# Kernel optimization log

Measured on AMD Instinct MI355X. Metric: run time of the kernel, lower is better.

Reference implementation:

```python
import jax, jax.numpy as jnp
import numpy as np

TEMP = 0.07
EPS = 1e-8
NUM_CLASSES = 7
THRESH = 0.3


def setup_inputs() -> dict:
    key = jax.random.key(0)
    k1, k2, k3, k4, k5 = jax.random.split(key, 5)
    N, H, E, C = 8192, 128, 256, NUM_CLASSES
    reps = jax.random.normal(k1, (N, H), dtype=jnp.float32)
    labels = jax.random.randint(k2, (N,), 0, C, dtype=jnp.int64 if jax.config.jax_enable_x64 else jnp.int32)
    centers = jax.random.normal(k3, (C, E), dtype=jnp.float32)
    fc_w = jax.random.normal(k4, (H, E), dtype=jnp.float32) * (1.0 / np.sqrt(E))
    fc_b = jax.random.normal(k5, (H,), dtype=jnp.float32) * 0.01
    return {"reps": reps, "labels": labels, "centers": centers, "fc_w": fc_w, "fc_b": fc_b}


def reference(reps, labels, centers, fc_w, fc_b):
    # fc(default_centers): [C, H]
    curr_centers = centers @ fc_w.T + fc_b
    pad_labels = jnp.arange(NUM_CLASSES, dtype=labels.dtype)

    all_reps = jnp.concatenate([reps, curr_centers], axis=0)      # [M, H]
    all_labels = jnp.concatenate([labels, pad_labels], axis=0)    # [M]
    B = reps.shape[0]
    M = all_reps.shape[0]

    # cosine similarity via normalized matmul (avoids [B,M,H] broadcast)
    norms = jnp.sqrt(jnp.sum(all_reps * all_reps, axis=-1))
    rn = all_reps / jnp.maximum(norms, 1e-8)[:, None]
    cos = rn[:B] @ rn.T                                           # [B, M]

    scores = (1.0 + cos) * 0.5 + EPS
    eye = (jnp.arange(B)[:, None] == jnp.arange(M)[None, :]).astype(scores.dtype)
    scores = scores * (1.0 - eye) / TEMP
    # torch uses .item() on the max -> a non-differentiable constant
    scores = scores - jax.lax.stop_gradient(jnp.max(scores))
    e = jnp.exp(scores)

    pos_mask = (labels[:, None] == all_labels[None, :]).astype(scores.dtype)  # [B, M]
    mask = 1.0 - eye

    pos_sum = jnp.sum(e * pos_mask * mask, axis=-1)
    neg_sum = jnp.sum(e * (1.0 - pos_mask), axis=-1)
    probs = pos_sum / (pos_sum + neg_sum)
    probs = probs / (jnp.sum(pos_mask * mask, axis=-1) + EPS)

    loss_vec = -jnp.log(probs + EPS)
    loss_mask = (loss_vec > THRESH).astype(loss_vec.dtype)
    denom = jax.lax.stop_gradient(jnp.sum(loss_mask)) + EPS
    loss = jnp.sum(loss_vec * loss_mask) / denom
    return loss
```

## Files before the change

### kernel.cpp

```cpp
#include <hip/hip_runtime.h>
#include <hip/hip_bf16.h>

#define BN 8192
#define MM 8199
#define MP 8208
#define HH 128
#define EE 256
#define GX2 64
#define GY 16
#define NUM_HIST 7

typedef __attribute__((ext_vector_type(8))) short short8;
typedef __attribute__((ext_vector_type(4))) float floatx4;


__global__ __launch_bounds__(256)
void prep_kernel(const float* __restrict__ reps,
                 const int* __restrict__ labels,
                 const float* __restrict__ centers,
                 const float* __restrict__ fc_w,
                 const float* __restrict__ fc_b,
                 __hip_bfloat16* __restrict__ rnt,
                 int* __restrict__ labp,
                 float* __restrict__ tot) {
  const int wid = threadIdx.x >> 6, lane = threadIdx.x & 63;
  const int b = blockIdx.x;
  if (b < 2048) {
    if (threadIdx.x < 8) tot[b * 8 + threadIdx.x] = 0.f;
    const int r = b * 4 + wid;
    float2 v = ((const float2*)(reps + (size_t)r * HH))[lane];
    float ss = v.x * v.x + v.y * v.y;
#pragma unroll
    for (int m = 1; m < 64; m <<= 1) ss += __shfl_xor(ss, m);
    float inv = 1.0f / fmaxf(sqrtf(ss), 1e-8f);
    __hip_bfloat162 h2;
    h2.x = __float2bfloat16(v.x * inv);
    h2.y = __float2bfloat16(v.y * inv);
    size_t o = (size_t)(r >> 4) * 1024 + (lane >> 2) * 64 + (r & 15) * 4 + (lane & 3);
    ((__hip_bfloat162*)rnt)[o] = h2;
    if (lane == 0) labp[r] = labels[r];
  } else {
    __shared__ float currs[7 * HH];
    for (int o = threadIdx.x; o < 7 * HH; o += 256) {
      int c = o >> 7, h = o & 127;
      const float4* ce = (const float4*)(centers + c * EE);
      const float4* w  = (const float4*)(fc_w + h * EE);
      float s = 0.f;
#pragma unroll 4
      for (int j = 0; j < EE / 4; ++j) {
        float4 a = ce[j], bb = w[j];
        s += a.x * bb.x + a.y * bb.y + a.z * bb.z + a.w * bb.w;
      }
      currs[o] = s + fc_b[h];
    }
    __syncthreads();
    for (int k = 0; k < 4; ++k) {
      int c = wid * 4 + k;
      int r = BN + c;
      float2 v = make_float2(0.f, 0.f);
      if (c < 7) v = ((const float2*)(currs + c * HH))[lane];
      float ss = v.x * v.x + v.y * v.y;
#pragma unroll
      for (int m = 1; m < 64; m <<= 1) ss += __shfl_xor(ss, m);
      float inv = 1.0f / fmaxf(sqrtf(ss), 1e-8f);
      __hip_bfloat162 h2;
      h2.x = __float2bfloat16(v.x * inv);
      h2.y = __float2bfloat16(v.y * inv);
      size_t o = (size_t)(r >> 4) * 1024 + (lane >> 2) * 64 + (r & 15) * 4 + (lane & 3);
      ((__hip_bfloat162*)rnt)[o] = h2;
      if (lane == 0) labp[r] = (r < MM) ? r - BN : -1;
    }
  }
}

__global__ __launch_bounds__(256, 2)
void main_kernel(const __hip_bfloat16* __restrict__ rnt,
                 const int* __restrict__ labp,
                 float* __restrict__ tot,
                 float* __restrict__ pos) {
  __shared__ short lbuf[2][4096];
  const int lane = threadIdx.x & 63;
  const int w    = threadIdx.x >> 6;
  const int q = lane >> 4, col = lane & 15;
  const int ibase = blockIdx.x * 128;
  const short* rns = (const short*)rnt;

  short8 afrag[2][4];
  int tix[2];
#pragma unroll
  for (int it = 0; it < 2; ++it) {
    tix[it] = blockIdx.x * 8 + w * 2 + it;
    const short* base = rns + (size_t)tix[it] * 2048 + lane * 8;
    afrag[it][0] = *(const short8*)(base);
    afrag[it][1] = *(const short8*)(base + 512);
    afrag[it][2] = *(const short8*)(base + 1024);
    afrag[it][3] = *(const short8*)(base + 1536);
  }
  int labi[2][4];
#pragma unroll
  for (int it = 0; it < 2; ++it)
#pragma unroll
    for (int r = 0; r < 4; ++r)
      labi[it][r] = labp[ibase + (w * 2 + it) * 16 + q * 4 + r];

  float stot[2][4] = {};
  float spos[2][4] = {};
  const float K2 = 10.30496147f;

  auto accum = [&](short8 b0, short8 b1, short8 b2, short8 b3, int t, int labj) {
#pragma unroll
    for (int it = 0; it < 2; ++it) {
      floatx4 acc = {0.f, 0.f, 0.f, 0.f};
      acc = __builtin_amdgcn_mfma_f32_16x16x32_bf16(afrag[it][0], b0, acc, 0, 0, 0);
      acc = __builtin_amdgcn_mfma_f32_16x16x32_bf16(afrag[it][1], b1, acc, 0, 0, 0);
      acc = __builtin_amdgcn_mfma_f32_16x16x32_bf16(afrag[it][2], b2, acc, 0, 0, 0);
      acc = __builtin_amdgcn_mfma_f32_16x16x32_bf16(afrag[it][3], b3, acc, 0, 0, 0);
      float ev[4];
#pragma unroll
      for (int r = 0; r < 4; ++r) {
        float e = __builtin_amdgcn_exp2f(fmaf(acc[r], K2, -K2));
        ev[r] = e;
        stot[it][r] += e;
        spos[it][r] += (labj == labi[it][r]) ? e : 0.f;
      }
      if (t == tix[it]) {
#pragma unroll
        for (int r = 0; r < 4; ++r)
          if (col == q * 4 + r) { stot[it][r] -= ev[r]; spos[it][r] -= ev[r]; }
      }
    }
  };

  const int t0 = blockIdx.y * 32;

  {
    const short* g = rns + (size_t)t0 * 2048 + threadIdx.x * 8;
    *(short8*)&lbuf[0][threadIdx.x * 8] = *(const short8*)g;
    *(short8*)&lbuf[0][2048 + threadIdx.x * 8] = *(const short8*)(g + 2048);
  }
  __syncthreads();

  for (int p = 0; p < 16; ++p) {
    const int cur = p & 1;
    const int t = t0 + p * 2;
    short8 nv0, nv1;
    const bool more = (p < 15);
    if (more) {
      const short* g = rns + (size_t)(t + 2) * 2048 + threadIdx.x * 8;
      nv0 = *(const short8*)g;
      nv1 = *(const short8*)(g + 2048);
    }
    const int labj0 = labp[t * 16 + col];
    const int labj1 = labp[t * 16 + 16 + col];

    const short* lb = &lbuf[cur][0];
    short8 b0 = *(const short8*)(lb + lane * 8);
    short8 b1 = *(const short8*)(lb + 512 + lane * 8);
    short8 b2 = *(const short8*)(lb + 1024 + lane * 8);
    short8 b3 = *(const short8*)(lb + 1536 + lane * 8);
    short8 c0 = *(const short8*)(lb + 2048 + lane * 8);
    short8 c1 = *(const short8*)(lb + 2560 + lane * 8);
    short8 c2 = *(const short8*)(lb + 3072 + lane * 8);
    short8 c3 = *(const short8*)(lb + 3584 + lane * 8);

    accum(b0, b1, b2, b3, t, labj0);
    accum(c0, c1, c2, c3, t + 1, labj1);

    if (more) {
      *(short8*)&lbuf[cur ^ 1][threadIdx.x * 8] = nv0;
      *(short8*)&lbuf[cur ^ 1][2048 + threadIdx.x * 8] = nv1;
    }
    __syncthreads();
  }

  if (blockIdx.y == GY - 1) {
    const short* g = rns + (size_t)512 * 2048 + lane * 8;
    short8 b0 = *(const short8*)(g);
    short8 b1 = *(const short8*)(g + 512);
    short8 b2 = *(const short8*)(g + 1024);
    short8 b3 = *(const short8*)(g + 1536);
    accum(b0, b1, b2, b3, 512, labp[512 * 16 + col]);
  }

#pragma unroll
  for (int it = 0; it < 2; ++it)
#pragma unroll
    for (int r = 0; r < 4; ++r) {
      float tt = stot[it][r], pp = spos[it][r];
#pragma unroll
      for (int m = 1; m <= 8; m <<= 1) {
        tt += __shfl_xor(tt, m);
        pp += __shfl_xor(pp, m);
      }
      if (col == 0) {
        int i = ibase + (w * 2 + it) * 16 + q * 4 + r;
        atomicAdd(&tot[i], tt);
        atomicAdd(&pos[i], pp);
      }
    }
}

__global__ __launch_bounds__(1024)
void loss_kernel(const float* __restrict__ tot,
                 const float* __restrict__ pos,
                 const int* __restrict__ labels,
                 float* __restrict__ out) {
  __shared__ int hist[NUM_HIST];
  __shared__ float s1[16], s2[16];
  const int tid = threadIdx.x;
  const int lane = tid & 63, wid = tid >> 6;
  if (tid < NUM_HIST) hist[tid] = 0;
  __syncthreads();
  int c0 = 0, c1 = 0, c2 = 0, c3 = 0, c4 = 0, c5 = 0, c6 = 0;
  for (int i = tid; i < BN; i += 1024) {
    int lab = labels[i];
    unsigned long long m0 = __ballot(lab == 0);
    unsigned long long m1 = __ballot(lab == 1);
    unsigned long long m2 = __ballot(lab == 2);
    unsigned long long m3 = __ballot(lab == 3);
    unsigned long long m4 = __ballot(lab == 4);
    unsigned long long m5 = __ballot(lab == 5);
    unsigned long long m6 = __ballot(lab == 6);
    if (lane == 0) {
      c0 += __popcll(m0); c1 += __popcll(m1); c2 += __popcll(m2);
      c3 += __popcll(m3); c4 += __popcll(m4); c5 += __popcll(m5);
      c6 += __popcll(m6);
    }
  }
  if (lane == 0) {
    atomicAdd(&hist[0], c0); atomicAdd(&hist[1], c1); atomicAdd(&hist[2], c2);
    atomicAdd(&hist[3], c3); atomicAdd(&hist[4], c4); atomicAdd(&hist[5], c5);
    atomicAdd(&hist[6], c6);
  }
  __syncthreads();
  const float K2 = 10.30496147f;
  const float epad9 = 9.0f * exp2f(-K2);
  float lsum = 0.f, msum = 0.f;
  for (int i = tid; i < BN; i += 1024) {
    float t = tot[i] - epad9;
    float p = pos[i];
    float c = (float)hist[labels[i]];
    float pr = (p / t) / (c + 1e-8f);
    float lv = -logf(pr + 1e-8f);
    if (lv > 0.3f) { lsum += lv; msum += 1.f; }
  }
#pragma unroll
  for (int m = 1; m < 64; m <<= 1) {
    lsum += __shfl_xor(lsum, m);
    msum += __shfl_xor(msum, m);
  }
  if (lane == 0) { s1[wid] = lsum; s2[wid] = msum; }
  __syncthreads();
  if (wid == 0) {
    float a = (lane < 16) ? s1[lane] : 0.f;
    float b = (lane < 16) ? s2[lane] : 0.f;
#pragma unroll
    for (int m = 1; m < 16; m <<= 1) {
      a += __shfl_xor(a, m);
      b += __shfl_xor(b, m);
    }
    if (lane == 0) out[0] = a / (b + 1e-8f);
  }
}

extern "C" void kernel_launch(void* const* d_in, const int* in_sizes, int n_in,
                              void* d_out, int out_size, void* d_ws, size_t ws_size,
                              hipStream_t stream) {
  const float* reps    = (const float*)d_in[0];
  const int*   labels  = (const int*)d_in[1];
  const float* centers = (const float*)d_in[2];
  const float* fc_w    = (const float*)d_in[3];
  const float* fc_b    = (const float*)d_in[4];
  float* out = (float*)d_out;

  char* ws = (char*)d_ws;
  int* labp   = (int*)(ws + 4096);
  __hip_bfloat16* rnt = (__hip_bfloat16*)(ws + 40960);
  float* tot = (float*)(ws + 40960 + 2101248);
  float* pos = tot + BN;

  prep_kernel<<<2049, 256, 0, stream>>>(reps, labels, centers, fc_w, fc_b, rnt, labp, tot);
  main_kernel<<<dim3(GX2, GY), 256, 0, stream>>>(rnt, labp, tot, pos);
  loss_kernel<<<1, 1024, 0, stream>>>(tot, pos, labels, out);
}
```

Measured before the change: 131.1 us.

## Exploit symmetry of the similarity matrix via triangular block tiling

The main kernel now walks only the upper-triangular 128x128 tiles of the B×B cosine matrix: 2080 blocks, each decoded from a linear index into (I,J). Off-diagonal tiles also accumulate column sums through shared-memory atomics and add them to the J rows, which roughly halves the MFMA and exp work. The cost is extra LDS atomics, shuffles and global atomics per tile. The grid becomes much finer, with only 4 loop iterations per block, so per-block setup (A-fragment loads, prologue) is amortised over less work. Reusing column sums is valid here because the label-equality mask is also symmetric.

```diff
diff --git a/kernel.cpp b/kernel.cpp
--- a/kernel.cpp
+++ b/kernel.cpp
@@ -6,8 +6,8 @@
 #define MP 8208
 #define HH 128
 #define EE 256
-#define GX2 64
-#define GY 16
+#define TSUP 64
+#define NTRI 2080
 #define NUM_HIST 7
 
 typedef __attribute__((ext_vector_type(8))) short short8;
@@ -79,17 +79,27 @@
                  float* __restrict__ tot,
                  float* __restrict__ pos) {
   __shared__ short lbuf[2][4096];
+  __shared__ float redc[256];
   const int lane = threadIdx.x & 63;
   const int w    = threadIdx.x >> 6;
   const int q = lane >> 4, col = lane & 15;
-  const int ibase = blockIdx.x * 128;
   const short* rns = (const short*)rnt;
+
+  const int idx = blockIdx.x;
+  int I = (int)(64.5f - sqrtf(4160.25f - 2.0f * (float)idx));
+  I = (I < 0) ? 0 : ((I > TSUP - 1) ? TSUP - 1 : I);
+  while (I * TSUP - (I * (I - 1)) / 2 > idx) --I;
+  while ((I + 1) * TSUP - ((I + 1) * I) / 2 <= idx) ++I;
+  const int J = I + (idx - (I * TSUP - (I * (I - 1)) / 2));
+  const bool offdiag = (I != J);
+
+  redc[threadIdx.x] = 0.f;
 
   short8 afrag[2][4];
   int tix[2];
 #pragma unroll
   for (int it = 0; it < 2; ++it) {
-    tix[it] = blockIdx.x * 8 + w * 2 + it;
+    tix[it] = I * 8 + w * 2 + it;
     const short* base = rns + (size_t)tix[it] * 2048 + lane * 8;
     afrag[it][0] = *(const short8*)(base);
     afrag[it][1] = *(const short8*)(base + 512);
@@ -101,13 +111,14 @@
   for (int it = 0; it < 2; ++it)
 #pragma unroll
     for (int r = 0; r < 4; ++r)
-      labi[it][r] = labp[ibase + (w * 2 + it) * 16 + q * 4 + r];
+      labi[it][r] = labp[tix[it] * 16 + q * 4 + r];
 
   float stot[2][4] = {};
   float spos[2][4] = {};
   const float K2 = 10.30496147f;
 
-  auto accum = [&](short8 b0, short8 b1, short8 b2, short8 b3, int t, int labj) {
+  auto accum = [&](short8 b0, short8 b1, short8 b2, short8 b3, int t, int labj,
+                   float* ct, float* cp) {
 #pragma unroll
     for (int it = 0; it < 2; ++it) {
       floatx4 acc = {0.f, 0.f, 0.f, 0.f};
@@ -120,8 +131,10 @@
       for (int r = 0; r < 4; ++r) {
         float e = __builtin_amdgcn_exp2f(fmaf(acc[r], K2, -K2));
         ev[r] = e;
+        float m = (labj == labi[it][r]) ? e : 0.f;
         stot[it][r] += e;
-        spos[it][r] += (labj == labi[it][r]) ? e : 0.f;
+        spos[it][r] += m;
+        if (ct) { *ct += e; *cp += m; }
       }
       if (t == tix[it]) {
 #pragma unroll
@@ -131,7 +144,7 @@
     }
   };
 
-  const int t0 = blockIdx.y * 32;
+  const int t0 = J * 8;
 
   {
     const short* g = rns + (size_t)t0 * 2048 + threadIdx.x * 8;
@@ -140,11 +153,11 @@
   }
   __syncthreads();
 
-  for (int p = 0; p < 16; ++p) {
+  for (int p = 0; p < 4; ++p) {
     const int cur = p & 1;
     const int t = t0 + p * 2;
     short8 nv0, nv1;
-    const bool more = (p < 15);
+    const bool more = (p < 3);
     if (more) {
       const short* g = rns + (size_t)(t + 2) * 2048 + threadIdx.x * 8;
       nv0 = *(const short8*)g;
@@ -154,17 +167,26 @@
     const int labj1 = labp[t * 16 + 16 + col];
 
     const short* lb = &lbuf[cur][0];
-    short8 b0 = *(const short8*)(lb + lane * 8);
-    short8 b1 = *(const short8*)(lb + 512 + lane * 8);
-    short8 b2 = *(const short8*)(lb + 1024 + lane * 8);
-    short8 b3 = *(const short8*)(lb + 1536 + lane * 8);
-    short8 c0 = *(const short8*)(lb + 2048 + lane * 8);
-    short8 c1 = *(const short8*)(lb + 2560 + lane * 8);
-    short8 c2 = *(const short8*)(lb + 3072 + lane * 8);
-    short8 c3 = *(const short8*)(lb + 3584 + lane * 8);
-
-    accum(b0, b1, b2, b3, t, labj0);
-    accum(c0, c1, c2, c3, t + 1, labj1);
+#pragma unroll
+    for (int u = 0; u < 2; ++u) {
+      const short* s = lb + u * 2048;
+      short8 b0 = *(const short8*)(s + lane * 8);
+      short8 b1 = *(const short8*)(s + 512 + lane * 8);
+      short8 b2 = *(const short8*)(s + 1024 + lane * 8);
+      short8 b3 = *(const short8*)(s + 1536 + lane * 8);
+      float ct = 0.f, cp = 0.f;
+      accum(b0, b1, b2, b3, t + u, u ? labj1 : labj0,
+            offdiag ? &ct : nullptr, offdiag ? &cp : nullptr);
+      if (offdiag) {
+        ct += __shfl_xor(ct, 16); ct += __shfl_xor(ct, 32);
+        cp += __shfl_xor(cp, 16); cp += __shfl_xor(cp, 32);
+        if (q == 0) {
+          int cj = (p * 2 + u) * 16 + col;
+          atomicAdd(&redc[cj], ct);
+          atomicAdd(&redc[128 + cj], cp);
+        }
+      }
+    }
 
     if (more) {
       *(short8*)&lbuf[cur ^ 1][threadIdx.x * 8] = nv0;
@@ -173,13 +195,13 @@
     __syncthreads();
   }
 
-  if (blockIdx.y == GY - 1) {
+  if (!offdiag) {
     const short* g = rns + (size_t)512 * 2048 + lane * 8;
     short8 b0 = *(const short8*)(g);
     short8 b1 = *(const short8*)(g + 512);
     short8 b2 = *(const short8*)(g + 1024);
     short8 b3 = *(const short8*)(g + 1536);
-    accum(b0, b1, b2, b3, 512, labp[512 * 16 + col]);
+    accum(b0, b1, b2, b3, 512, labp[512 * 16 + col], nullptr, nullptr);
   }
 
 #pragma unroll
@@ -193,11 +215,18 @@
         pp += __shfl_xor(pp, m);
       }
       if (col == 0) {
-        int i = ibase + (w * 2 + it) * 16 + q * 4 + r;
+        int i = tix[it] * 16 + q * 4 + r;
         atomicAdd(&tot[i], tt);
         atomicAdd(&pos[i], pp);
       }
     }
+
+  if (offdiag) {
+    if (threadIdx.x < 128)
+      atomicAdd(&tot[J * 128 + threadIdx.x], redc[threadIdx.x]);
+    else
+      atomicAdd(&pos[J * 128 + threadIdx.x - 128], redc[threadIdx.x]);
+  }
 }
 
 __global__ __launch_bounds__(1024)
@@ -280,6 +309,6 @@
   float* pos = tot + BN;
 
   prep_kernel<<<2049, 256, 0, stream>>>(reps, labels, centers, fc_w, fc_b, rnt, labp, tot);
-  main_kernel<<<dim3(GX2, GY), 256, 0, stream>>>(rnt, labp, tot, pos);
+  main_kernel<<<NTRI, 256, 0, stream>>>(rnt, labp, tot, pos);
   loss_kernel<<<1, 1024, 0, stream>>>(tot, pos, labels, out);
 }
```

New measurement: 187.0 us. 1.43x slower.
